# Kernel tuning notes

Hardware: AMD Instinct MI355X
Metric: run time of the kernel (lower is better)

The kernel has to match this reference:

```python
import jax, jax.numpy as jnp
import numpy as np

MAX_SEQ_LENGTH = 32
LN_EPS = 1e-5


def setup_inputs() -> dict:
    key = jax.random.key(0)
    ks = jax.random.split(key, 6)
    N, T, D, H, O = 256, 1024, 128, 256, 128
    G = 4 * H
    # torch kaiming_normal_ on a 2D (in, 4H) tensor: fan_in = size(1) = 4H, std = sqrt(2/fan_in)
    std_k = float(np.sqrt(2.0 / G))
    X = jax.random.normal(ks[0], (N, T, D), dtype=jnp.float32)
    Wx = jax.random.normal(ks[1], (D, G), dtype=jnp.float32) * std_k
    Wh = jax.random.normal(ks[2], (H, G), dtype=jnp.float32) * std_k
    b = jnp.zeros((G,), dtype=jnp.float32)
    W1 = jax.random.normal(ks[3], (H, H), dtype=jnp.float32) * float(np.sqrt(1.0 / H))
    b1 = jnp.zeros((H,), dtype=jnp.float32)
    ln_gamma = jnp.ones((H,), dtype=jnp.float32)
    ln_beta = jnp.zeros((H,), dtype=jnp.float32)
    W2 = jax.random.normal(ks[4], (H, O), dtype=jnp.float32) * float(np.sqrt(1.0 / H))
    b2 = jnp.zeros((O,), dtype=jnp.float32)
    return {"X": X, "Wx": Wx, "Wh": Wh, "b": b, "W1": W1, "b1": b1,
            "ln_gamma": ln_gamma, "ln_beta": ln_beta, "W2": W2, "b2": b2}


def _fc(h, W1, b1, ln_gamma, ln_beta, W2, b2):
    z = h @ W1 + b1
    mu = jnp.mean(z, axis=-1, keepdims=True)
    var = jnp.var(z, axis=-1, keepdims=True)
    z = (z - mu) * jax.lax.rsqrt(var + LN_EPS) * ln_gamma + ln_beta
    z = jax.nn.relu(z)
    return z @ W2 + b2


def reference(X, Wx, Wh, b, W1, b1, ln_gamma, ln_beta, W2, b2):
    N, T, D = X.shape
    H = Wh.shape[0]
    h0 = jnp.zeros((N, H), dtype=X.dtype)
    c0 = jnp.zeros((N, H), dtype=X.dtype)

    # --- encoder: standard LSTM cell (sigmoid/tanh gates) ---
    def enc_step(carry, x_t):
        h, c = carry
        fm = x_t @ Wx + h @ Wh + b  # (N, 4H)
        i = jax.nn.sigmoid(fm[:, 0:H])
        f = jax.nn.sigmoid(fm[:, H:2 * H])
        o = jax.nn.sigmoid(fm[:, 2 * H:3 * H])
        g = jnp.tanh(fm[:, 3 * H:4 * H])
        c = c * f + i * g
        h = o * jnp.tanh(c)
        return (h, c), None

    (h, c), _ = jax.lax.scan(enc_step, (h0, c0), jnp.swapaxes(X, 0, 1))

    # --- decoder: NOTE original code uses RAW gate slices (no sigmoid/tanh),
    # and start_token is zeros so the start_token @ Wx term is exactly 0. ---
    def dec_step(carry, _):
        h, c = carry
        fm = h @ Wh + b  # zeros @ Wx contributes 0
        i = fm[:, 0:H]
        f = fm[:, H:2 * H]
        o = fm[:, 2 * H:3 * H]
        g = fm[:, 3 * H:4 * H]
        c = c * f + i * g
        h = o * jnp.tanh(c)
        y = _fc(h, W1, b1, ln_gamma, ln_beta, W2, b2)
        return (h, c), y

    _, ys = jax.lax.scan(dec_step, (h, c), None, length=MAX_SEQ_LENGTH)
    return jnp.swapaxes(ys, 0, 1)  # (N, max_seq_length, output_dim)
```

## Files before the change

kernel.cpp:

```cpp
#include <hip/hip_runtime.h>
#include <cmath>

typedef _Float16 f16;
typedef _Float16 f16x4v __attribute__((ext_vector_type(4)));
typedef _Float16 f16x8v __attribute__((ext_vector_type(8)));
typedef float f32x4v __attribute__((ext_vector_type(4)));

#define NTHR 256
#define WPG  16

__device__ __forceinline__ float sigmoidf_(float x) { return 1.0f / (1.0f + expf(-x)); }

__device__ __forceinline__ void store_sc(float* p, float v) {
  asm volatile("global_store_dword %0, %1, off sc0 sc1" :: "v"(p), "v"(v) : "memory");
}

__device__ __forceinline__ void ld4_sc(const float* p,
                                       float4& a, float4& b, float4& c, float4& d) {
  asm volatile(
      "global_load_dwordx4 %0, %4, off sc0 sc1\n\t"
      "global_load_dwordx4 %1, %5, off sc0 sc1\n\t"
      "global_load_dwordx4 %2, %6, off sc0 sc1\n\t"
      "global_load_dwordx4 %3, %7, off sc0 sc1\n\t"
      "s_waitcnt vmcnt(0)"
      : "=&v"(a), "=&v"(b), "=&v"(c), "=&v"(d)
      : "v"(p), "v"(p + 1024), "v"(p + 2048), "v"(p + 3072)
      : "memory");
}

__device__ __forceinline__ void arrive_bar(unsigned* cg) {
  asm volatile("s_waitcnt vmcnt(0)" ::: "memory");
  __syncthreads();
  if (threadIdx.x == 0)
    (void)__hip_atomic_fetch_add(cg, 1u, __ATOMIC_RELAXED, __HIP_MEMORY_SCOPE_AGENT);
}

__device__ __forceinline__ void wait_bar(unsigned* cg, unsigned target) {
  if (threadIdx.x == 0) {
    unsigned guard = 0;
    while (__hip_atomic_load(cg, __ATOMIC_RELAXED, __HIP_MEMORY_SCOPE_AGENT) < target) {
      __builtin_amdgcn_s_sleep(1);
      if (++guard > (1u << 22)) break;
    }
  }
  __syncthreads();
}

__device__ __forceinline__ void conv4_wr(float4 v, f16* ph, f16* pl) {
  f16x4v h, l;
  h[0] = (f16)v.x; h[1] = (f16)v.y; h[2] = (f16)v.z; h[3] = (f16)v.w;
  l[0] = (f16)(v.x - (float)h[0]); l[1] = (f16)(v.y - (float)h[1]);
  l[2] = (f16)(v.z - (float)h[2]); l[3] = (f16)(v.w - (float)h[3]);
  *(f16x4v*)ph = h; *(f16x4v*)pl = l;
}

__device__ __forceinline__ void conv8_wr(float4 a, float4 b, f16* ph, f16* pl) {
  f16x8v h, l;
  h[0]=(f16)a.x; h[1]=(f16)a.y; h[2]=(f16)a.z; h[3]=(f16)a.w;
  h[4]=(f16)b.x; h[5]=(f16)b.y; h[6]=(f16)b.z; h[7]=(f16)b.w;
  l[0]=(f16)(a.x-(float)h[0]); l[1]=(f16)(a.y-(float)h[1]);
  l[2]=(f16)(a.z-(float)h[2]); l[3]=(f16)(a.w-(float)h[3]);
  l[4]=(f16)(b.x-(float)h[4]); l[5]=(f16)(b.y-(float)h[5]);
  l[6]=(f16)(b.z-(float)h[6]); l[7]=(f16)(b.w-(float)h[7]);
  *(f16x8v*)ph = h; *(f16x8v*)pl = l;
}

__global__ __launch_bounds__(NTHR, 1) void lstm_k(
    const float* __restrict__ X,  const float* __restrict__ Wx,
    const float* __restrict__ Wh, const float* __restrict__ Bg,
    const float* __restrict__ W1, const float* __restrict__ B1,
    const float* __restrict__ LNG, const float* __restrict__ LNB,
    const float* __restrict__ W2, const float* __restrict__ B2,
    float* __restrict__ Y, unsigned* __restrict__ CNT,
    float* __restrict__ hbuf, float* __restrict__ zbuf)
{
  __shared__ f16   A_hi[16][392];
  __shared__ f16   A_lo[16][392];
  __shared__ float fm_lds[16][65];
  __shared__ float hst[16][264];
  __shared__ float w1_lds[16][268];
  __shared__ float w2_lds[8][268];
  __shared__ float lng_lds[256], lnb_lds[256];
  __shared__ float ln_mu[16], ln_rs[16];

  const int tid = threadIdx.x;
  const int wg  = blockIdx.x;
  const int g   = wg & 15;
  const int jm  = wg >> 4;
  const int n0  = g * 16;
  const int k0  = jm * 16;
  unsigned* cg  = CNT + g * 32;

  const int l     = tid & 63;
  const int w     = __builtin_amdgcn_readfirstlane(tid >> 6);
  const int krow0 = (l >> 4) * 8;
  const int arow  = l & 15;

  f16x8v Bh[12], Bl[12];
  {
    const int bcol = w * 256 + k0 + (l & 15);
    #pragma unroll
    for (int kt = 0; kt < 12; ++kt) {
      #pragma unroll
      for (int j = 0; j < 8; ++j) {
        int k = kt * 32 + krow0 + j;
        float v = (kt < 4) ? Wx[k * 1024 + bcol] : Wh[(k - 128) * 1024 + bcol];
        f16 hi = (f16)v;
        Bh[kt][j] = hi;
        Bl[kt][j] = (f16)(v - (float)hi);
      }
    }
  }

  for (int idx = tid; idx < 256 * 16; idx += NTHR) {
    int k = idx >> 4, cc = idx & 15;
    w1_lds[cc][k] = W1[k * 256 + k0 + cc];
  }
  for (int idx = tid; idx < 256 * 8; idx += NTHR) {
    int k = idx >> 3, cc = idx & 7;
    w2_lds[cc][k] = W2[k * 128 + jm * 8 + cc];
  }
  lng_lds[tid] = LNG[tid];
  lnb_lds[tid] = LNB[tid];

  const int gr = tid >> 4, gk = tid & 15;
  const float bias0 = Bg[      k0 + gk];
  const float bias1 = Bg[256 + k0 + gk];
  const float bias2 = Bg[512 + k0 + gk];
  const float bias3 = Bg[768 + k0 + gk];
  const float b1reg = B1[k0 + gk];
  const float b2reg = (tid < 128) ? B2[jm * 8 + (tid & 7)] : 0.0f;
  float c_reg = 0.0f;

  {
    const float* xp = X + (size_t)(n0 + (tid >> 4)) * 131072 + (size_t)(tid & 15) * 8;
    float4 xa = *(const float4*)xp;
    float4 xb = *(const float4*)(xp + 4);
    conv8_wr(xa, xb, &A_hi[tid >> 4][(tid & 15) * 8], &A_lo[tid >> 4][(tid & 15) * 8]);
    f16x8v z8 = {0,0,0,0,0,0,0,0};
    *(f16x8v*)&A_hi[tid >> 4][128 + (tid & 15) * 16] = z8;
    *(f16x8v*)&A_hi[tid >> 4][136 + (tid & 15) * 16] = z8;
    *(f16x8v*)&A_lo[tid >> 4][128 + (tid & 15) * 16] = z8;
    *(f16x8v*)&A_lo[tid >> 4][136 + (tid & 15) * 16] = z8;
  }
  __syncthreads();

  auto stage_h_A = [&](const float* hs) {
    float4 v0, v1, v2, v3;
    ld4_sc(hs, v0, v1, v2, v3);
    conv4_wr(v0, &A_hi[w     ][128 + 4 * l], &A_lo[w     ][128 + 4 * l]);
    conv4_wr(v1, &A_hi[w + 4 ][128 + 4 * l], &A_lo[w + 4 ][128 + 4 * l]);
    conv4_wr(v2, &A_hi[w + 8 ][128 + 4 * l], &A_lo[w + 8 ][128 + 4 * l]);
    conv4_wr(v3, &A_hi[w + 12][128 + 4 * l], &A_lo[w + 12][128 + 4 * l]);
  };

  for (int t = 0; t < 1024; ++t) {
    float4 xa, xb;
    if (t < 1023) {
      const float* xp = X + (size_t)(n0 + (tid >> 4)) * 131072
                          + (size_t)(t + 1) * 128 + (size_t)(tid & 15) * 8;
      xa = *(const float4*)xp;
      xb = *(const float4*)(xp + 4);
    }

    f16x8v ah[12], al[12];
    {
      const f16* pah = &A_hi[arow][krow0];
      const f16* pal = &A_lo[arow][krow0];
      #pragma unroll
      for (int kt = 0; kt < 12; ++kt) {
        ah[kt] = *(const f16x8v*)(pah + kt * 32);
        al[kt] = *(const f16x8v*)(pal + kt * 32);
      }
    }
    f32x4v ac0 = {0,0,0,0}, ac1 = {0,0,0,0}, ac2 = {0,0,0,0};
    #pragma unroll
    for (int kt = 0; kt < 12; ++kt) {
      ac0 = __builtin_amdgcn_mfma_f32_16x16x32_f16(ah[kt], Bh[kt], ac0, 0, 0, 0);
      ac1 = __builtin_amdgcn_mfma_f32_16x16x32_f16(ah[kt], Bl[kt], ac1, 0, 0, 0);
      ac2 = __builtin_amdgcn_mfma_f32_16x16x32_f16(al[kt], Bh[kt], ac2, 0, 0, 0);
    }
    #pragma unroll
    for (int q = 0; q < 4; ++q)
      fm_lds[(l >> 4) * 4 + q][w * 16 + (l & 15)] = ac0[q] + ac1[q] + ac2[q];
    __syncthreads();

    {
      float fi = fm_lds[gr][     gk] + bias0;
      float ff = fm_lds[gr][16 + gk] + bias1;
      float fo = fm_lds[gr][32 + gk] + bias2;
      float fg = fm_lds[gr][48 + gk] + bias3;
      float si = sigmoidf_(fi), sf = sigmoidf_(ff), so = sigmoidf_(fo);
      float tg = tanhf(fg);
      c_reg = c_reg * sf + si * tg;
      float hv = so * tanhf(c_reg);
      store_sc(hbuf + (size_t)(t & 1) * 65536 + (size_t)(n0 + gr) * 256 + k0 + gk, hv);
    }

    if (t < 1023)
      conv8_wr(xa, xb, &A_hi[tid >> 4][(tid & 15) * 8], &A_lo[tid >> 4][(tid & 15) * 8]);

    arrive_bar(cg);
    if (t < 1023) {
      wait_bar(cg, (unsigned)(WPG * (t + 1)));
      stage_h_A(hbuf + (size_t)(t & 1) * 65536 + (size_t)n0 * 256 + (size_t)tid * 4);
      __syncthreads();
    }
  }

  wait_bar(cg, (unsigned)(WPG * 1024));
  stage_h_A(hbuf + (size_t)65536  + (size_t)n0 * 256 + (size_t)tid * 4);
  __syncthreads();
  unsigned arr = 1024;

  for (int s = 0; s < 32; ++s) {
    const int t = 1024 + s;

    f16x8v ah[8], al[8];
    {
      const f16* pah = &A_hi[arow][128 + krow0];
      const f16* pal = &A_lo[arow][128 + krow0];
      #pragma unroll
      for (int kt = 0; kt < 8; ++kt) {
        ah[kt] = *(const f16x8v*)(pah + kt * 32);
        al[kt] = *(const f16x8v*)(pal + kt * 32);
      }
    }
    f32x4v ac0 = {0,0,0,0}, ac1 = {0,0,0,0}, ac2 = {0,0,0,0};
    #pragma unroll
    for (int kt = 0; kt < 8; ++kt) {
      ac0 = __builtin_amdgcn_mfma_f32_16x16x32_f16(ah[kt], Bh[kt + 4], ac0, 0, 0, 0);
      ac1 = __builtin_amdgcn_mfma_f32_16x16x32_f16(ah[kt], Bl[kt + 4], ac1, 0, 0, 0);
      ac2 = __builtin_amdgcn_mfma_f32_16x16x32_f16(al[kt], Bh[kt + 4], ac2, 0, 0, 0);
    }
    #pragma unroll
    for (int q = 0; q < 4; ++q)
      fm_lds[(l >> 4) * 4 + q][w * 16 + (l & 15)] = ac0[q] + ac1[q] + ac2[q];
    __syncthreads();

    {
      float fi = fm_lds[gr][     gk] + bias0;
      float ff = fm_lds[gr][16 + gk] + bias1;
      float fo = fm_lds[gr][32 + gk] + bias2;
      float fg = fm_lds[gr][48 + gk] + bias3;
      c_reg = c_reg * ff + fi * fg;
      float hv = fo * tanhf(c_reg);
      store_sc(hbuf + (size_t)(t & 1) * 65536 + (size_t)(n0 + gr) * 256 + k0 + gk, hv);
    }
    arrive_bar(cg); ++arr;
    wait_bar(cg, WPG * arr);

    {
      const float* hs = hbuf + (size_t)(t & 1) * 65536 + (size_t)n0 * 256 + (size_t)tid * 4;
      float4 v0, v1, v2, v3;
      ld4_sc(hs, v0, v1, v2, v3);
      *(float4*)&hst[w     ][4 * l] = v0;
      *(float4*)&hst[w + 4 ][4 * l] = v1;
      *(float4*)&hst[w + 8 ][4 * l] = v2;
      *(float4*)&hst[w + 12][4 * l] = v3;
      conv4_wr(v0, &A_hi[w     ][128 + 4 * l], &A_lo[w     ][128 + 4 * l]);
      conv4_wr(v1, &A_hi[w + 4 ][128 + 4 * l], &A_lo[w + 4 ][128 + 4 * l]);
      conv4_wr(v2, &A_hi[w + 8 ][128 + 4 * l], &A_lo[w + 8 ][128 + 4 * l]);
      conv4_wr(v3, &A_hi[w + 12][128 + 4 * l], &A_lo[w + 12][128 + 4 * l]);
    }
    __syncthreads();

    {
      float za = b1reg;
      const float* hr = &hst[gr][0];
      const float* wr = &w1_lds[gk][0];
      #pragma unroll 4
      for (int kc = 0; kc < 64; ++kc) {
        float4 h4 = *(const float4*)(hr + kc * 4);
        float4 w4 = *(const float4*)(wr + kc * 4);
        za = fmaf(h4.x, w4.x, fmaf(h4.y, w4.y, fmaf(h4.z, w4.z, fmaf(h4.w, w4.w, za))));
      }
      store_sc(zbuf + (size_t)(n0 + gr) * 256 + k0 + gk, za);
    }
    arrive_bar(cg); ++arr;
    wait_bar(cg, WPG * arr);

    {
      const float* zs = zbuf + (size_t)n0 * 256 + (size_t)tid * 4;
      float4 v0, v1, v2, v3;
      ld4_sc(zs, v0, v1, v2, v3);
      *(float4*)&hst[w     ][4 * l] = v0;
      *(float4*)&hst[w + 4 ][4 * l] = v1;
      *(float4*)&hst[w + 8 ][4 * l] = v2;
      *(float4*)&hst[w + 12][4 * l] = v3;
    }
    __syncthreads();

    {
      const float* zr = &hst[gr][0];
      float s1 = 0.f, s2 = 0.f;
      #pragma unroll
      for (int u = 0; u < 16; ++u) { float v = zr[gk * 16 + u]; s1 += v; s2 += v * v; }
      #pragma unroll
      for (int d = 1; d < 16; d <<= 1) { s1 += __shfl_xor(s1, d); s2 += __shfl_xor(s2, d); }
      float mu = s1 * (1.0f / 256.0f);
      float var = s2 * (1.0f / 256.0f) - mu * mu;
      float rstd = rsqrtf(var + 1e-5f);
      if (gk == 0) { ln_mu[gr] = mu; ln_rs[gr] = rstd; }
    }
    __syncthreads();

    #pragma unroll
    for (int rep = 0; rep < 4; ++rep) {
      int f = tid + 256 * rep, r = f >> 6, kq = f & 63;
      float mu = ln_mu[r], rs = ln_rs[r];
      float4 v = *(float4*)&hst[r][kq * 4];
      int cb = kq * 4;
      v.x = fmaxf(fmaf((v.x - mu) * rs, lng_lds[cb    ], lnb_lds[cb    ]), 0.f);
      v.y = fmaxf(fmaf((v.y - mu) * rs, lng_lds[cb + 1], lnb_lds[cb + 1]), 0.f);
      v.z = fmaxf(fmaf((v.z - mu) * rs, lng_lds[cb + 2], lnb_lds[cb + 2]), 0.f);
      v.w = fmaxf(fmaf((v.w - mu) * rs, lng_lds[cb + 3], lnb_lds[cb + 3]), 0.f);
      *(float4*)&hst[r][kq * 4] = v;
    }
    __syncthreads();

    if (tid < 128) {
      int r = tid >> 3, yc = tid & 7;
      float ya = b2reg;
      const float* zr = &hst[r][0];
      const float* wr = &w2_lds[yc][0];
      #pragma unroll 4
      for (int kc = 0; kc < 64; ++kc) {
        float4 z4 = *(const float4*)(zr + kc * 4);
        float4 w4 = *(const float4*)(wr + kc * 4);
        ya = fmaf(z4.x, w4.x, fmaf(z4.y, w4.y, fmaf(z4.z, w4.z, fmaf(z4.w, w4.w, ya))));
      }
      Y[(size_t)(n0 + r) * 4096 + (size_t)s * 128 + jm * 8 + yc] = ya;
    }
  }
}

extern "C" void kernel_launch(void* const* d_in, const int* in_sizes, int n_in,
                              void* d_out, int out_size, void* d_ws, size_t ws_size,
                              hipStream_t stream) {
  const float* X   = (const float*)d_in[0];
  const float* Wx  = (const float*)d_in[1];
  const float* Wh  = (const float*)d_in[2];
  const float* b   = (const float*)d_in[3];
  const float* W1  = (const float*)d_in[4];
  const float* b1  = (const float*)d_in[5];
  const float* lng = (const float*)d_in[6];
  const float* lnb = (const float*)d_in[7];
  const float* W2  = (const float*)d_in[8];
  const float* b2  = (const float*)d_in[9];
  float* Y = (float*)d_out;

  unsigned* cnt = (unsigned*)d_ws;
  float* hbuf = (float*)((char*)d_ws + 2048);
  float* zbuf = hbuf + 2 * 256 * 256;
  (void)in_sizes; (void)n_in; (void)out_size; (void)ws_size;

  hipMemsetAsync(d_ws, 0, 2048, stream);
  hipLaunchKernelGGL(lstm_k, dim3(256), dim3(NTHR), 0, stream,
                     X, Wx, Wh, b, W1, b1, lng, lnb, W2, b2, Y, cnt, hbuf, zbuf);
}
```

Before: 2.964 ms.

## Replace counter barriers with tagged value flags and split MFMA K across waves

The per-group atomic counter barrier is replaced by storing each h/z value together with a step tag in a 64-bit word. Consumers poll their own 16-element slice until every tag matches, which removes the separate arrive/wait round trip and the thread-0 spin plus block sync. The MFMA work is also redistributed so each wave covers a K-slice across all four gate groups and partial sums are reduced through LDS. This costs more workspace, a larger memset and wider loads, and makes every thread spin on global memory.

```diff
diff --git a/kernel.cpp b/kernel.cpp
--- a/kernel.cpp
+++ b/kernel.cpp
@@ -2,56 +2,59 @@
 #include <cmath>
 
 typedef _Float16 f16;
-typedef _Float16 f16x4v __attribute__((ext_vector_type(4)));
 typedef _Float16 f16x8v __attribute__((ext_vector_type(8)));
 typedef float f32x4v __attribute__((ext_vector_type(4)));
+typedef unsigned long long u64;
 
 #define NTHR 256
-#define WPG  16
 
 __device__ __forceinline__ float sigmoidf_(float x) { return 1.0f / (1.0f + expf(-x)); }
 
-__device__ __forceinline__ void store_sc(float* p, float v) {
-  asm volatile("global_store_dword %0, %1, off sc0 sc1" :: "v"(p), "v"(v) : "memory");
-}
-
-__device__ __forceinline__ void ld4_sc(const float* p,
-                                       float4& a, float4& b, float4& c, float4& d) {
+__device__ __forceinline__ void store_pair(u64* p, float v, unsigned tag) {
+  u64 u = (u64)__float_as_uint(v) | ((u64)tag << 32);
+  asm volatile("global_store_dwordx2 %0, %1, off sc0 sc1" :: "v"(p), "v"(u) : "memory");
+}
+
+__device__ __forceinline__ void ld8_sc(const u64* p,
+    float4& c0, float4& c1, float4& c2, float4& c3,
+    float4& c4, float4& c5, float4& c6, float4& c7) {
   asm volatile(
-      "global_load_dwordx4 %0, %4, off sc0 sc1\n\t"
-      "global_load_dwordx4 %1, %5, off sc0 sc1\n\t"
-      "global_load_dwordx4 %2, %6, off sc0 sc1\n\t"
-      "global_load_dwordx4 %3, %7, off sc0 sc1\n\t"
+      "global_load_dwordx4 %0, %8, off sc0 sc1\n\t"
+      "global_load_dwordx4 %1, %8, off offset:16 sc0 sc1\n\t"
+      "global_load_dwordx4 %2, %8, off offset:32 sc0 sc1\n\t"
+      "global_load_dwordx4 %3, %8, off offset:48 sc0 sc1\n\t"
+      "global_load_dwordx4 %4, %8, off offset:64 sc0 sc1\n\t"
+      "global_load_dwordx4 %5, %8, off offset:80 sc0 sc1\n\t"
+      "global_load_dwordx4 %6, %8, off offset:96 sc0 sc1\n\t"
+      "global_load_dwordx4 %7, %8, off offset:112 sc0 sc1\n\t"
       "s_waitcnt vmcnt(0)"
-      : "=&v"(a), "=&v"(b), "=&v"(c), "=&v"(d)
-      : "v"(p), "v"(p + 1024), "v"(p + 2048), "v"(p + 3072)
+      : "=&v"(c0), "=&v"(c1), "=&v"(c2), "=&v"(c3),
+        "=&v"(c4), "=&v"(c5), "=&v"(c6), "=&v"(c7)
+      : "v"(p)
       : "memory");
 }
 
-__device__ __forceinline__ void arrive_bar(unsigned* cg) {
-  asm volatile("s_waitcnt vmcnt(0)" ::: "memory");
-  __syncthreads();
-  if (threadIdx.x == 0)
-    (void)__hip_atomic_fetch_add(cg, 1u, __ATOMIC_RELAXED, __HIP_MEMORY_SCOPE_AGENT);
-}
-
-__device__ __forceinline__ void wait_bar(unsigned* cg, unsigned target) {
-  if (threadIdx.x == 0) {
-    unsigned guard = 0;
-    while (__hip_atomic_load(cg, __ATOMIC_RELAXED, __HIP_MEMORY_SCOPE_AGENT) < target) {
-      __builtin_amdgcn_s_sleep(1);
-      if (++guard > (1u << 22)) break;
-    }
-  }
-  __syncthreads();
-}
-
-__device__ __forceinline__ void conv4_wr(float4 v, f16* ph, f16* pl) {
-  f16x4v h, l;
-  h[0] = (f16)v.x; h[1] = (f16)v.y; h[2] = (f16)v.z; h[3] = (f16)v.w;
-  l[0] = (f16)(v.x - (float)h[0]); l[1] = (f16)(v.y - (float)h[1]);
-  l[2] = (f16)(v.z - (float)h[2]); l[3] = (f16)(v.w - (float)h[3]);
-  *(f16x4v*)ph = h; *(f16x4v*)pl = l;
+__device__ __forceinline__ void poll16(const u64* p, unsigned want, float* out) {
+  float4 c0, c1, c2, c3, c4, c5, c6, c7;
+  unsigned guard = 0;
+  for (;;) {
+    ld8_sc(p, c0, c1, c2, c3, c4, c5, c6, c7);
+    bool ok = (__float_as_uint(c0.y) == want) && (__float_as_uint(c0.w) == want)
+           && (__float_as_uint(c1.y) == want) && (__float_as_uint(c1.w) == want)
+           && (__float_as_uint(c2.y) == want) && (__float_as_uint(c2.w) == want)
+           && (__float_as_uint(c3.y) == want) && (__float_as_uint(c3.w) == want)
+           && (__float_as_uint(c4.y) == want) && (__float_as_uint(c4.w) == want)
+           && (__float_as_uint(c5.y) == want) && (__float_as_uint(c5.w) == want)
+           && (__float_as_uint(c6.y) == want) && (__float_as_uint(c6.w) == want)
+           && (__float_as_uint(c7.y) == want) && (__float_as_uint(c7.w) == want);
+    if (ok) break;
+    if (++guard > (1u << 22)) break;
+    __builtin_amdgcn_s_sleep(1);
+  }
+  out[0]  = c0.x; out[1]  = c0.z; out[2]  = c1.x; out[3]  = c1.z;
+  out[4]  = c2.x; out[5]  = c2.z; out[6]  = c3.x; out[7]  = c3.z;
+  out[8]  = c4.x; out[9]  = c4.z; out[10] = c5.x; out[11] = c5.z;
+  out[12] = c6.x; out[13] = c6.z; out[14] = c7.x; out[15] = c7.z;
 }
 
 __device__ __forceinline__ void conv8_wr(float4 a, float4 b, f16* ph, f16* pl) {
@@ -65,19 +68,29 @@
   *(f16x8v*)ph = h; *(f16x8v*)pl = l;
 }
 
+__device__ __forceinline__ void conv16_wr(const float* v, f16* ph, f16* pl) {
+  f16x8v h0, h1, l0, l1;
+  #pragma unroll
+  for (int j = 0; j < 8; ++j) {
+    h0[j] = (f16)v[j];     l0[j] = (f16)(v[j]     - (float)h0[j]);
+    h1[j] = (f16)v[8 + j]; l1[j] = (f16)(v[8 + j] - (float)h1[j]);
+  }
+  *(f16x8v*)ph = h0; *(f16x8v*)(ph + 8) = h1;
+  *(f16x8v*)pl = l0; *(f16x8v*)(pl + 8) = l1;
+}
+
 __global__ __launch_bounds__(NTHR, 1) void lstm_k(
     const float* __restrict__ X,  const float* __restrict__ Wx,
     const float* __restrict__ Wh, const float* __restrict__ Bg,
     const float* __restrict__ W1, const float* __restrict__ B1,
     const float* __restrict__ LNG, const float* __restrict__ LNB,
     const float* __restrict__ W2, const float* __restrict__ B2,
-    float* __restrict__ Y, unsigned* __restrict__ CNT,
-    float* __restrict__ hbuf, float* __restrict__ zbuf)
+    float* __restrict__ Y, u64* __restrict__ HP, u64* __restrict__ ZP)
 {
   __shared__ f16   A_hi[16][392];
   __shared__ f16   A_lo[16][392];
-  __shared__ float fm_lds[16][65];
-  __shared__ float hst[16][264];
+  __shared__ float fm_p[4][64][20];
+  __shared__ float hst[16][260];
   __shared__ float w1_lds[16][268];
   __shared__ float w2_lds[8][268];
   __shared__ float lng_lds[256], lnb_lds[256];
@@ -89,25 +102,29 @@
   const int jm  = wg >> 4;
   const int n0  = g * 16;
   const int k0  = jm * 16;
-  unsigned* cg  = CNT + g * 32;
 
   const int l     = tid & 63;
   const int w     = __builtin_amdgcn_readfirstlane(tid >> 6);
+  const int lr    = l & 15;
   const int krow0 = (l >> 4) * 8;
-  const int arow  = l & 15;
-
-  f16x8v Bh[12], Bl[12];
-  {
-    const int bcol = w * 256 + k0 + (l & 15);
-    #pragma unroll
-    for (int kt = 0; kt < 12; ++kt) {
+
+  const int srow = tid & 15;
+  const int scb  = tid >> 4;
+
+  f16x8v Bh[3][4], Bl[3][4];
+  #pragma unroll
+  for (int ki = 0; ki < 3; ++ki) {
+    const int kt = w + 4 * ki;
+    #pragma unroll
+    for (int n = 0; n < 4; ++n) {
+      const int gcol = n * 256 + k0 + lr;
       #pragma unroll
       for (int j = 0; j < 8; ++j) {
         int k = kt * 32 + krow0 + j;
-        float v = (kt < 4) ? Wx[k * 1024 + bcol] : Wh[(k - 128) * 1024 + bcol];
+        float v = (k < 128) ? Wx[k * 1024 + gcol] : Wh[(k - 128) * 1024 + gcol];
         f16 hi = (f16)v;
-        Bh[kt][j] = hi;
-        Bl[kt][j] = (f16)(v - (float)hi);
+        Bh[ki][n][j] = hi;
+        Bl[ki][n][j] = (f16)(v - (float)hi);
       }
     }
   }
@@ -133,135 +150,136 @@
   float c_reg = 0.0f;
 
   {
-    const float* xp = X + (size_t)(n0 + (tid >> 4)) * 131072 + (size_t)(tid & 15) * 8;
+    f16x8v z8 = {0, 0, 0, 0, 0, 0, 0, 0};
+    *(f16x8v*)&A_hi[srow][128 + scb * 16]     = z8;
+    *(f16x8v*)&A_hi[srow][128 + scb * 16 + 8] = z8;
+    *(f16x8v*)&A_lo[srow][128 + scb * 16]     = z8;
+    *(f16x8v*)&A_lo[srow][128 + scb * 16 + 8] = z8;
+    const float* xp = X + (size_t)(n0 + srow) * 131072 + (size_t)scb * 8;
     float4 xa = *(const float4*)xp;
     float4 xb = *(const float4*)(xp + 4);
-    conv8_wr(xa, xb, &A_hi[tid >> 4][(tid & 15) * 8], &A_lo[tid >> 4][(tid & 15) * 8]);
-    f16x8v z8 = {0,0,0,0,0,0,0,0};
-    *(f16x8v*)&A_hi[tid >> 4][128 + (tid & 15) * 16] = z8;
-    *(f16x8v*)&A_hi[tid >> 4][136 + (tid & 15) * 16] = z8;
-    *(f16x8v*)&A_lo[tid >> 4][128 + (tid & 15) * 16] = z8;
-    *(f16x8v*)&A_lo[tid >> 4][136 + (tid & 15) * 16] = z8;
+    conv8_wr(xa, xb, &A_hi[srow][scb * 8], &A_lo[srow][scb * 8]);
   }
   __syncthreads();
 
-  auto stage_h_A = [&](const float* hs) {
-    float4 v0, v1, v2, v3;
-    ld4_sc(hs, v0, v1, v2, v3);
-    conv4_wr(v0, &A_hi[w     ][128 + 4 * l], &A_lo[w     ][128 + 4 * l]);
-    conv4_wr(v1, &A_hi[w + 4 ][128 + 4 * l], &A_lo[w + 4 ][128 + 4 * l]);
-    conv4_wr(v2, &A_hi[w + 8 ][128 + 4 * l], &A_lo[w + 8 ][128 + 4 * l]);
-    conv4_wr(v3, &A_hi[w + 12][128 + 4 * l], &A_lo[w + 12][128 + 4 * l]);
-  };
-
   for (int t = 0; t < 1024; ++t) {
-    float4 xa, xb;
-    if (t < 1023) {
-      const float* xp = X + (size_t)(n0 + (tid >> 4)) * 131072
-                          + (size_t)(t + 1) * 128 + (size_t)(tid & 15) * 8;
-      xa = *(const float4*)xp;
-      xb = *(const float4*)(xp + 4);
-    }
-
-    f16x8v ah[12], al[12];
-    {
-      const f16* pah = &A_hi[arow][krow0];
-      const f16* pal = &A_lo[arow][krow0];
-      #pragma unroll
-      for (int kt = 0; kt < 12; ++kt) {
-        ah[kt] = *(const f16x8v*)(pah + kt * 32);
-        al[kt] = *(const f16x8v*)(pal + kt * 32);
-      }
-    }
-    f32x4v ac0 = {0,0,0,0}, ac1 = {0,0,0,0}, ac2 = {0,0,0,0};
-    #pragma unroll
-    for (int kt = 0; kt < 12; ++kt) {
-      ac0 = __builtin_amdgcn_mfma_f32_16x16x32_f16(ah[kt], Bh[kt], ac0, 0, 0, 0);
-      ac1 = __builtin_amdgcn_mfma_f32_16x16x32_f16(ah[kt], Bl[kt], ac1, 0, 0, 0);
-      ac2 = __builtin_amdgcn_mfma_f32_16x16x32_f16(al[kt], Bh[kt], ac2, 0, 0, 0);
-    }
-    #pragma unroll
-    for (int q = 0; q < 4; ++q)
-      fm_lds[(l >> 4) * 4 + q][w * 16 + (l & 15)] = ac0[q] + ac1[q] + ac2[q];
-    __syncthreads();
-
-    {
-      float fi = fm_lds[gr][     gk] + bias0;
-      float ff = fm_lds[gr][16 + gk] + bias1;
-      float fo = fm_lds[gr][32 + gk] + bias2;
-      float fg = fm_lds[gr][48 + gk] + bias3;
+    f16x8v axh = *(const f16x8v*)&A_hi[lr][w * 32 + krow0];
+    f16x8v axl = *(const f16x8v*)&A_lo[lr][w * 32 + krow0];
+    f16x8v ah1 = *(const f16x8v*)&A_hi[lr][128 + w * 32 + krow0];
+    f16x8v al1 = *(const f16x8v*)&A_lo[lr][128 + w * 32 + krow0];
+    f16x8v ah2 = *(const f16x8v*)&A_hi[lr][128 + (w + 4) * 32 + krow0];
+    f16x8v al2 = *(const f16x8v*)&A_lo[lr][128 + (w + 4) * 32 + krow0];
+
+    f32x4v ac0[4], ac1[4], ac2[4];
+    #pragma unroll
+    for (int n = 0; n < 4; ++n) { ac0[n] = {0,0,0,0}; ac1[n] = {0,0,0,0}; ac2[n] = {0,0,0,0}; }
+    #pragma unroll
+    for (int n = 0; n < 4; ++n) {
+      ac0[n] = __builtin_amdgcn_mfma_f32_16x16x32_f16(axh, Bh[0][n], ac0[n], 0, 0, 0);
+      ac1[n] = __builtin_amdgcn_mfma_f32_16x16x32_f16(axh, Bl[0][n], ac1[n], 0, 0, 0);
+      ac2[n] = __builtin_amdgcn_mfma_f32_16x16x32_f16(axl, Bh[0][n], ac2[n], 0, 0, 0);
+      ac0[n] = __builtin_amdgcn_mfma_f32_16x16x32_f16(ah1, Bh[1][n], ac0[n], 0, 0, 0);
+      ac1[n] = __builtin_amdgcn_mfma_f32_16x16x32_f16(ah1, Bl[1][n], ac1[n], 0, 0, 0);
+      ac2[n] = __builtin_amdgcn_mfma_f32_16x16x32_f16(al1, Bh[1][n], ac2[n], 0, 0, 0);
+      ac0[n] = __builtin_amdgcn_mfma_f32_16x16x32_f16(ah2, Bh[2][n], ac0[n], 0, 0, 0);
+      ac1[n] = __builtin_amdgcn_mfma_f32_16x16x32_f16(ah2, Bl[2][n], ac1[n], 0, 0, 0);
+      ac2[n] = __builtin_amdgcn_mfma_f32_16x16x32_f16(al2, Bh[2][n], ac2[n], 0, 0, 0);
+    }
+    #pragma unroll
+    for (int n = 0; n < 4; ++n) {
+      f32x4v s = ac0[n] + ac1[n] + ac2[n];
+      *(f32x4v*)&fm_p[w][n * 16 + lr][(l >> 4) * 4] = s;
+    }
+    __syncthreads();
+
+    {
+      float fi = bias0, ff = bias1, fo = bias2, fg = bias3;
+      #pragma unroll
+      for (int ww = 0; ww < 4; ++ww) {
+        fi += fm_p[ww][     gk][gr];
+        ff += fm_p[ww][16 + gk][gr];
+        fo += fm_p[ww][32 + gk][gr];
+        fg += fm_p[ww][48 + gk][gr];
+      }
       float si = sigmoidf_(fi), sf = sigmoidf_(ff), so = sigmoidf_(fo);
       float tg = tanhf(fg);
       c_reg = c_reg * sf + si * tg;
       float hv = so * tanhf(c_reg);
-      store_sc(hbuf + (size_t)(t & 1) * 65536 + (size_t)(n0 + gr) * 256 + k0 + gk, hv);
-    }
-
-    if (t < 1023)
-      conv8_wr(xa, xb, &A_hi[tid >> 4][(tid & 15) * 8], &A_lo[tid >> 4][(tid & 15) * 8]);
-
-    arrive_bar(cg);
+      store_pair(HP + (size_t)(t & 1) * 65536 + (size_t)(n0 + gr) * 256 + k0 + gk,
+                 hv, (unsigned)(t + 1));
+    }
+
     if (t < 1023) {
-      wait_bar(cg, (unsigned)(WPG * (t + 1)));
-      stage_h_A(hbuf + (size_t)(t & 1) * 65536 + (size_t)n0 * 256 + (size_t)tid * 4);
-      __syncthreads();
-    }
-  }
-
-  wait_bar(cg, (unsigned)(WPG * 1024));
-  stage_h_A(hbuf + (size_t)65536  + (size_t)n0 * 256 + (size_t)tid * 4);
+      const float* xp = X + (size_t)(n0 + srow) * 131072 + (size_t)(t + 1) * 128
+                          + (size_t)scb * 8;
+      float4 xa = *(const float4*)xp;
+      float4 xb = *(const float4*)(xp + 4);
+      conv8_wr(xa, xb, &A_hi[srow][scb * 8], &A_lo[srow][scb * 8]);
+      float hv16[16];
+      poll16(HP + (size_t)(t & 1) * 65536 + (size_t)(n0 + srow) * 256 + scb * 16,
+             (unsigned)(t + 1), hv16);
+      conv16_wr(hv16, &A_hi[srow][128 + scb * 16], &A_lo[srow][128 + scb * 16]);
+    }
+    __syncthreads();
+  }
+
+  {
+    float hv16[16];
+    poll16(HP + (size_t)65536 + (size_t)(n0 + srow) * 256 + scb * 16, 1024u, hv16);
+    conv16_wr(hv16, &A_hi[srow][128 + scb * 16], &A_lo[srow][128 + scb * 16]);
+  }
   __syncthreads();
-  unsigned arr = 1024;
 
   for (int s = 0; s < 32; ++s) {
     const int t = 1024 + s;
 
-    f16x8v ah[8], al[8];
-    {
-      const f16* pah = &A_hi[arow][128 + krow0];
-      const f16* pal = &A_lo[arow][128 + krow0];
-      #pragma unroll
-      for (int kt = 0; kt < 8; ++kt) {
-        ah[kt] = *(const f16x8v*)(pah + kt * 32);
-        al[kt] = *(const f16x8v*)(pal + kt * 32);
-      }
-    }
-    f32x4v ac0 = {0,0,0,0}, ac1 = {0,0,0,0}, ac2 = {0,0,0,0};
-    #pragma unroll
-    for (int kt = 0; kt < 8; ++kt) {
-      ac0 = __builtin_amdgcn_mfma_f32_16x16x32_f16(ah[kt], Bh[kt + 4], ac0, 0, 0, 0);
-      ac1 = __builtin_amdgcn_mfma_f32_16x16x32_f16(ah[kt], Bl[kt + 4], ac1, 0, 0, 0);
-      ac2 = __builtin_amdgcn_mfma_f32_16x16x32_f16(al[kt], Bh[kt + 4], ac2, 0, 0, 0);
-    }
-    #pragma unroll
-    for (int q = 0; q < 4; ++q)
-      fm_lds[(l >> 4) * 4 + q][w * 16 + (l & 15)] = ac0[q] + ac1[q] + ac2[q];
-    __syncthreads();
-
-    {
-      float fi = fm_lds[gr][     gk] + bias0;
-      float ff = fm_lds[gr][16 + gk] + bias1;
-      float fo = fm_lds[gr][32 + gk] + bias2;
-      float fg = fm_lds[gr][48 + gk] + bias3;
+    f16x8v ah1 = *(const f16x8v*)&A_hi[lr][128 + w * 32 + krow0];
+    f16x8v al1 = *(const f16x8v*)&A_lo[lr][128 + w * 32 + krow0];
+    f16x8v ah2 = *(const f16x8v*)&A_hi[lr][128 + (w + 4) * 32 + krow0];
+    f16x8v al2 = *(const f16x8v*)&A_lo[lr][128 + (w + 4) * 32 + krow0];
+
+    f32x4v ac0[4], ac1[4], ac2[4];
+    #pragma unroll
+    for (int n = 0; n < 4; ++n) { ac0[n] = {0,0,0,0}; ac1[n] = {0,0,0,0}; ac2[n] = {0,0,0,0}; }
+    #pragma unroll
+    for (int n = 0; n < 4; ++n) {
+      ac0[n] = __builtin_amdgcn_mfma_f32_16x16x32_f16(ah1, Bh[1][n], ac0[n], 0, 0, 0);
+      ac1[n] = __builtin_amdgcn_mfma_f32_16x16x32_f16(ah1, Bl[1][n], ac1[n], 0, 0, 0);
+      ac2[n] = __builtin_amdgcn_mfma_f32_16x16x32_f16(al1, Bh[1][n], ac2[n], 0, 0, 0);
+      ac0[n] = __builtin_amdgcn_mfma_f32_16x16x32_f16(ah2, Bh[2][n], ac0[n], 0, 0, 0);
+      ac1[n] = __builtin_amdgcn_mfma_f32_16x16x32_f16(ah2, Bl[2][n], ac1[n], 0, 0, 0);
+      ac2[n] = __builtin_amdgcn_mfma_f32_16x16x32_f16(al2, Bh[2][n], ac2[n], 0, 0, 0);
+    }
+    #pragma unroll
+    for (int n = 0; n < 4; ++n) {
+      f32x4v sum = ac0[n] + ac1[n] + ac2[n];
+      *(f32x4v*)&fm_p[w][n * 16 + lr][(l >> 4) * 4] = sum;
+    }
+    __syncthreads();
+
+    {
+      float fi = bias0, ff = bias1, fo = bias2, fg = bias3;
+      #pragma unroll
+      for (int ww = 0; ww < 4; ++ww) {
+        fi += fm_p[ww][     gk][gr];
+        ff += fm_p[ww][16 + gk][gr];
+        fo += fm_p[ww][32 + gk][gr];
+        fg += fm_p[ww][48 + gk][gr];
+      }
       c_reg = c_reg * ff + fi * fg;
       float hv = fo * tanhf(c_reg);
-      store_sc(hbuf + (size_t)(t & 1) * 65536 + (size_t)(n0 + gr) * 256 + k0 + gk, hv);
-    }
-    arrive_bar(cg); ++arr;
-    wait_bar(cg, WPG * arr);
-
-    {
-      const float* hs = hbuf + (size_t)(t & 1) * 65536 + (size_t)n0 * 256 + (size_t)tid * 4;
-      float4 v0, v1, v2, v3;
-      ld4_sc(hs, v0, v1, v2, v3);
-      *(float4*)&hst[w     ][4 * l] = v0;
-      *(float4*)&hst[w + 4 ][4 * l] = v1;
-      *(float4*)&hst[w + 8 ][4 * l] = v2;
-      *(float4*)&hst[w + 12][4 * l] = v3;
-      conv4_wr(v0, &A_hi[w     ][128 + 4 * l], &A_lo[w     ][128 + 4 * l]);
-      conv4_wr(v1, &A_hi[w + 4 ][128 + 4 * l], &A_lo[w + 4 ][128 + 4 * l]);
-      conv4_wr(v2, &A_hi[w + 8 ][128 + 4 * l], &A_lo[w + 8 ][128 + 4 * l]);
-      conv4_wr(v3, &A_hi[w + 12][128 + 4 * l], &A_lo[w + 12][128 + 4 * l]);
+      store_pair(HP + (size_t)(t & 1) * 65536 + (size_t)(n0 + gr) * 256 + k0 + gk,
+                 hv, (unsigned)(t + 1));
+    }
+
+    {
+      float hv16[16];
+      poll16(HP + (size_t)(t & 1) * 65536 + (size_t)(n0 + srow) * 256 + scb * 16,
+             (unsigned)(t + 1), hv16);
+      conv16_wr(hv16, &A_hi[srow][128 + scb * 16], &A_lo[srow][128 + scb * 16]);
+      #pragma unroll
+      for (int j = 0; j < 4; ++j)
+        *(float4*)&hst[srow][scb * 16 + 4 * j] = *(const float4*)&hv16[4 * j];
     }
     __syncthreads();
 
@@ -275,19 +293,16 @@
         float4 w4 = *(const float4*)(wr + kc * 4);
         za = fmaf(h4.x, w4.x, fmaf(h4.y, w4.y, fmaf(h4.z, w4.z, fmaf(h4.w, w4.w, za))));
       }
-      store_sc(zbuf + (size_t)(n0 + gr) * 256 + k0 + gk, za);
-    }
-    arrive_bar(cg); ++arr;
-    wait_bar(cg, WPG * arr);
-
-    {
-      const float* zs = zbuf + (size_t)n0 * 256 + (size_t)tid * 4;
-      float4 v0, v1, v2, v3;
-      ld4_sc(zs, v0, v1, v2, v3);
-      *(float4*)&hst[w     ][4 * l] = v0;
-      *(float4*)&hst[w + 4 ][4 * l] = v1;
-      *(float4*)&hst[w + 8 ][4 * l] = v2;
-      *(float4*)&hst[w + 12][4 * l] = v3;
+      store_pair(ZP + (size_t)(n0 + gr) * 256 + k0 + gk, za, (unsigned)(s + 1));
+    }
+    __syncthreads();
+
+    {
+      float hv16[16];
+      poll16(ZP + (size_t)(n0 + srow) * 256 + scb * 16, (unsigned)(s + 1), hv16);
+      #pragma unroll
+      for (int j = 0; j < 4; ++j)
+        *(float4*)&hst[srow][scb * 16 + 4 * j] = *(const float4*)&hv16[4 * j];
     }
     __syncthreads();
 
@@ -350,12 +365,11 @@
   const float* b2  = (const float*)d_in[9];
   float* Y = (float*)d_out;
 
-  unsigned* cnt = (unsigned*)d_ws;
-  float* hbuf = (float*)((char*)d_ws + 2048);
-  float* zbuf = hbuf + 2 * 256 * 256;
+  u64* HP = (u64*)d_ws;
+  u64* ZP = HP + 2 * 65536;
   (void)in_sizes; (void)n_in; (void)out_size; (void)ws_size;
 
-  hipMemsetAsync(d_ws, 0, 2048, stream);
+  hipMemsetAsync(d_ws, 0, 3 * 65536 * sizeof(u64), stream);
   hipLaunchKernelGGL(lstm_k, dim3(256), dim3(NTHR), 0, stream,
-                     X, Wx, Wh, b, W1, b1, lng, lnb, W2, b2, Y, cnt, hbuf, zbuf);
-}
+                     X, Wx, Wh, b, W1, b1, lng, lnb, W2, b2, Y, HP, ZP);
+}
```

Result: slower. 4.205 ms (+41.9%).
